# Kernel optimization log

Measured on AMD Instinct MI355X. Metric: run time of the kernel, lower is better.

## Reference

```python
import jax, jax.numpy as jnp
import numpy as np

N = 50000      # total batched graph nodes (both ASTs of all examples)
E = 30000      # edges per edge type
T = 8          # num edge types (no master node, no sibling edges)
H = 128        # gnn hidden = change_vector_dim // 2
TAG = 32       # change-tag embed size
CONTENT = H - TAG
VOCAB = 20000  # rows of token/content encoding table
B = 64         # num examples
STEPS = (3, 3) # layer_time_steps


def setup_inputs() -> dict:
    key = jax.random.key(0)
    ks = jax.random.split(key, 22)
    s = 0.05
    inp = {}
    inp["node_content_ids"] = jax.random.randint(ks[0], (N,), 0, VOCAB)
    inp["node_tag_ids"] = jax.random.randint(ks[1], (N,), 0, 4)
    inp["edge_src"] = jax.random.randint(ks[2], (T, E), 0, N)
    inp["edge_tgt"] = jax.random.randint(ks[3], (T, E), 0, N)
    inp["node2example"] = jnp.sort(jax.random.randint(ks[4], (N,), 0, B))
    inp["content_table"] = jax.random.normal(ks[5], (VOCAB, CONTENT)) * s
    inp["tag_embedding"] = jax.random.normal(ks[6], (4, TAG)) * s
    inp["msg_W"] = jax.random.normal(ks[7], (2, T, H, H)) * s
    inp["msg_b"] = jax.random.normal(ks[8], (2, T, H)) * s
    inp["gru0_Wih"] = jax.random.normal(ks[9], (H, 3 * H)) * s
    inp["gru0_Whh"] = jax.random.normal(ks[10], (H, 3 * H)) * s
    inp["gru0_bih"] = jax.random.normal(ks[11], (3 * H,)) * s
    inp["gru0_bhh"] = jax.random.normal(ks[12], (3 * H,)) * s
    inp["gru1_Wih"] = jax.random.normal(ks[13], (2 * H, 3 * H)) * s  # layer 1 gets residual concat -> 2H input
    inp["gru1_Whh"] = jax.random.normal(ks[14], (H, 3 * H)) * s
    inp["gru1_bih"] = jax.random.normal(ks[15], (3 * H,)) * s
    inp["gru1_bhh"] = jax.random.normal(ks[16], (3 * H,)) * s
    inp["r1_w"] = jax.random.normal(ks[17], (H,)) * s
    inp["r1_b"] = jax.random.normal(ks[18], ()) * s
    inp["r2_w"] = jax.random.normal(ks[19], (H,)) * s
    inp["r2_b"] = jax.random.normal(ks[20], ()) * s
    return inp


def _gru(x, h, Wih, Whh, bih, bhh):
    # PyTorch GRUCell gate order: r, z, n
    gi = x @ Wih + bih
    gh = h @ Whh + bhh
    i_r, i_z, i_n = jnp.split(gi, 3, axis=-1)
    h_r, h_z, h_n = jnp.split(gh, 3, axis=-1)
    r = jax.nn.sigmoid(i_r + h_r)
    z = jax.nn.sigmoid(i_z + h_z)
    n = jnp.tanh(i_n + r * h_n)
    return (1.0 - z) * n + z * h


def reference(node_content_ids, node_tag_ids, edge_src, edge_tgt, node2example,
              content_table, tag_embedding, msg_W, msg_b,
              gru0_Wih, gru0_Whh, gru0_bih, gru0_bhh,
              gru1_Wih, gru1_Whh, gru1_bih, gru1_bhh,
              r1_w, r1_b, r2_w, r2_b):
    # init node embeddings: [token/content encoding || change-tag embedding] -> [N, H]
    init = jnp.concatenate([content_table[node_content_ids],
                            tag_embedding[node_tag_ids]], axis=-1)
    states = init
    layer_out = []
    for layer, steps in enumerate(STEPS):
        for _ in range(steps):
            src_states = states[edge_src]                                   # [T,E,H] gather
            msgs = jnp.einsum('teh,thd->ted', src_states, msg_W[layer]) \
                   + msg_b[layer][:, None, :]                               # per-edge-type linear
            agg = jnp.zeros_like(states).at[edge_tgt].add(msgs)             # scatter-add to targets
            if layer == 1:
                # residual_connections={1:[0]}: concat initial states with incoming messages
                x = jnp.concatenate([init, agg], axis=-1)
                states = _gru(x, states, gru1_Wih, gru1_Whh, gru1_bih, gru1_bhh)
            else:
                states = _gru(agg, states, gru0_Wih, gru0_Whh, gru0_bih, gru0_bhh)
        layer_out.append(states)
    s1, s2 = layer_out
    # gated scalar readout per layer, pooled per example, concatenated -> [B, 2H]
    g1 = jax.nn.sigmoid(s1 @ r1_w + r1_b)[:, None]
    g2 = jax.nn.sigmoid(s2 @ r2_w + r2_b)[:, None]
    pooled1 = jax.ops.segment_sum(g1 * s1, node2example, num_segments=B)
    pooled2 = jax.ops.segment_sum(g2 * s2, node2example, num_segments=B)
    return jnp.concatenate([pooled1, pooled2], axis=-1)
```

## Files before the change

### kernel.cpp

```cpp
#include <hip/hip_runtime.h>
#include <hip/hip_bf16.h>

#define NN 50000
#define NE 30000
#define NT 8
#define HH 128
#define NB 64
#define CONT 96
#define TPB 16
#define EDGES (NT * NE)
#define SBLK 512
#define SNB ((NN + SBLK - 1) / SBLK)
#define RCH 8
#define NTILE (NN / 16)
#define NPAIR ((NTILE + 1) / 2)

typedef __attribute__((ext_vector_type(8))) short short8;
typedef __attribute__((ext_vector_type(4))) float f32x4;

__device__ __forceinline__ float sigm(float x) { return 1.f / (1.f + __expf(-x)); }
__device__ __forceinline__ unsigned short bfbits(float x) {
  __hip_bfloat16 b = __float2bfloat16(x);
  return *(unsigned short*)&b;
}

__global__ __launch_bounds__(256) void init_kernel(
    const int* __restrict__ cid, const int* __restrict__ tg,
    const float* __restrict__ ctab, const float* __restrict__ ttab,
    __hip_bfloat16* __restrict__ sbf, __hip_bfloat16* __restrict__ ibf)
{
  int i = blockIdx.x * 256 + threadIdx.x;
  if (i >= NN * HH) return;
  int n = i >> 7, d = i & 127;
  float v;
  if (d < CONT) v = ctab[(size_t)cid[n] * CONT + d];
  else          v = ttab[(size_t)tg[n] * 32 + (d - CONT)];
  __hip_bfloat16 b = __float2bfloat16(v);
  sbf[i] = b;
  ibf[i] = b;
}

__global__ __launch_bounds__(256) void hist_kernel(
    const int* __restrict__ etgt, int* __restrict__ cnt)
{
  int i = blockIdx.x * 256 + threadIdx.x;
  if (i >= EDGES) return;
  atomicAdd(&cnt[etgt[i]], 1);
}

__global__ __launch_bounds__(SBLK) void scanA_kernel(
    const int* __restrict__ cnt, int* __restrict__ row_ptr, int* __restrict__ bsum)
{
  __shared__ int sm[SBLK];
  const int tid = threadIdx.x;
  const int i = blockIdx.x * SBLK + tid;
  int v = (i < NN) ? cnt[i] : 0;
  sm[tid] = v;
  __syncthreads();
  for (int off = 1; off < SBLK; off <<= 1) {
    int t = (tid >= off) ? sm[tid - off] : 0;
    __syncthreads();
    sm[tid] += t;
    __syncthreads();
  }
  if (i < NN) row_ptr[i] = sm[tid] - v;
  if (tid == SBLK - 1) bsum[blockIdx.x] = sm[tid];
}

__global__ __launch_bounds__(128) void scanB_kernel(
    const int* __restrict__ bsum, int* __restrict__ boff, int* __restrict__ row_ptr)
{
  __shared__ int sm[128];
  const int tid = threadIdx.x;
  int v = (tid < SNB) ? bsum[tid] : 0;
  sm[tid] = v;
  __syncthreads();
  for (int off = 1; off < 128; off <<= 1) {
    int t = (tid >= off) ? sm[tid - off] : 0;
    __syncthreads();
    sm[tid] += t;
    __syncthreads();
  }
  if (tid < SNB) boff[tid] = sm[tid] - v;
  if (tid == 127) row_ptr[NN] = sm[127];
}

__global__ __launch_bounds__(SBLK) void scanC_kernel(
    int* __restrict__ row_ptr, int* __restrict__ cnt2, const int* __restrict__ boff)
{
  int i = blockIdx.x * SBLK + threadIdx.x;
  if (i >= NN) return;
  int r = row_ptr[i] + boff[blockIdx.x];
  row_ptr[i] = r;
  cnt2[i] = r;
}

__global__ __launch_bounds__(256) void scatter_kernel(
    const int* __restrict__ etgt, int* __restrict__ cnt2, int* __restrict__ perm)
{
  int i = blockIdx.x * 256 + threadIdx.x;
  if (i >= EDGES) return;
  perm[i] = atomicAdd(&cnt2[etgt[i]], 1);
}

__global__ __launch_bounds__(128) void exbound_kernel(
    const int* __restrict__ n2e, int* __restrict__ ebnd)
{
  int ex = threadIdx.x;
  if (ex > NB) return;
  int lo = 0, hi = NN;
  while (lo < hi) { int mid = (lo + hi) >> 1; if (n2e[mid] < ex) lo = mid + 1; else hi = mid; }
  ebnd[ex] = lo;
}

__device__ __forceinline__ void gru_swz_one(
    const float* __restrict__ W, __hip_bfloat16* __restrict__ out, int KSL, int mode, int i)
{
  int j = i & 7, lane = (i >> 3) & 63, kk = (i >> 9) % KSL, nt = i / (KSL * 512);
  int hi = lane >> 4, lo = lane & 15;
  int p = kk * 32 + hi * 8 + j;
  int k;
  if (mode == 0)      k = p;
  else if (mode == 1) k = (p & 7) * 16 + (p >> 3);
  else                k = (p < 128) ? p : 128 + ((p - 128) & 7) * 16 + ((p - 128) >> 3);
  out[i] = __float2bfloat16(W[(size_t)k * 384 + nt * 16 + lo]);
}

__global__ __launch_bounds__(256) void wswz_all_kernel(
    const float* __restrict__ msgW, __hip_bfloat16* __restrict__ wswz,
    const float* __restrict__ g0Wih, __hip_bfloat16* __restrict__ w0ih,
    const float* __restrict__ g0Whh, __hip_bfloat16* __restrict__ w0hh,
    const float* __restrict__ g1Wih, __hip_bfloat16* __restrict__ w1ih,
    const float* __restrict__ g1Whh, __hip_bfloat16* __restrict__ w1hh)
{
  int i = blockIdx.x * 256 + threadIdx.x;
  if (i < 262144) {
    int j = i & 7, lane = (i >> 3) & 63, kk = (i >> 9) & 3, nt = (i >> 11) & 7, lt = i >> 14;
    int hi = lane >> 4, lo = lane & 15;
    int k = kk * 32 + hi * 8 + j;
    wswz[i] = __float2bfloat16(msgW[((size_t)lt * HH + k) * HH + nt * 16 + lo]);
    return;
  }
  i -= 262144;
  if (i < 49152)  { gru_swz_one(g0Wih, w0ih, 4, 1, i); return; }
  i -= 49152;
  if (i < 49152)  { gru_swz_one(g0Whh, w0hh, 4, 0, i); return; }
  i -= 49152;
  if (i < 98304)  { gru_swz_one(g1Wih, w1ih, 8, 2, i); return; }
  i -= 98304;
  if (i < 49152)  { gru_swz_one(g1Whh, w1hh, 4, 0, i); return; }
}

__global__ __launch_bounds__(256) void msg_mfma_kernel(
    const __hip_bfloat16* __restrict__ sbf, const int* __restrict__ esrc,
    const int* __restrict__ perm, const __hip_bfloat16* __restrict__ wswz,
    const float* __restrict__ ball, __hip_bfloat16* __restrict__ msgs, int layer)
{
  __shared__ short8 Wl[8 * 4 * 64];
  const int t = blockIdx.y;
  {
    const float4* wg = (const float4*)(wswz + (size_t)(layer * NT + t) * 16384);
    float4* wl = (float4*)Wl;
    for (int i = threadIdx.x; i < 2048; i += 256) wl[i] = wg[i];
  }
  const int lane = threadIdx.x & 63;
  const int wv   = threadIdx.x >> 6;
  const int hi = lane >> 4, lo = lane & 15;
  float bias_v[8];
#pragma unroll
  for (int nt = 0; nt < 8; ++nt)
    bias_v[nt] = ball[(layer * NT + t) * HH + nt * 16 + lo];
  __syncthreads();

  const int tile_end = min((int)(blockIdx.x + 1) * TPB, NE / 16);
  for (int tile = blockIdx.x * TPB + wv; tile < tile_end; tile += 4) {
    const int e0 = tile * 16;
    const int src = esrc[t * NE + e0 + lo];
    const short* srow = (const short*)(sbf + (size_t)src * HH);
    short8 a[4];
#pragma unroll
    for (int kk = 0; kk < 4; ++kk)
      a[kk] = *(const short8*)(srow + kk * 32 + hi * 8);
    int slot[4];
#pragma unroll
    for (int r = 0; r < 4; ++r) slot[r] = perm[t * NE + e0 + hi * 4 + r];
    f32x4 acc[8];
#pragma unroll
    for (int nt = 0; nt < 8; ++nt) acc[nt] = (f32x4){0.f, 0.f, 0.f, 0.f};
#pragma unroll
    for (int nt = 0; nt < 8; ++nt)
#pragma unroll
      for (int kk = 0; kk < 4; ++kk)
        acc[nt] = __builtin_amdgcn_mfma_f32_16x16x32_bf16(
            a[kk], Wl[(nt * 4 + kk) * 64 + lane], acc[nt], 0, 0, 0);
#pragma unroll
    for (int r = 0; r < 4; ++r) {
      short8 m;
#pragma unroll
      for (int nt = 0; nt < 8; ++nt)
        ((unsigned short*)&m)[nt] = bfbits(acc[nt][r] + bias_v[nt]);
      *(short8*)((short*)msgs + (size_t)slot[r] * HH + lo * 8) = m;
    }
  }
}

__global__ __launch_bounds__(256) void reduce_kernel(
    const __hip_bfloat16* __restrict__ msgs, const int* __restrict__ row_ptr,
    __hip_bfloat16* __restrict__ agg)
{
  const int lane = threadIdx.x & 63;
  const int n = blockIdx.x * 4 + (threadIdx.x >> 6);
  if (n >= NN) return;
  const int b = row_ptr[n], e = row_ptr[n + 1];
  float a0 = 0.f, a1 = 0.f;
  for (int i = b; i < e; ++i) {
    unsigned int v = *(const unsigned int*)((const short*)msgs + (size_t)i * HH + lane * 2);
    a0 += __uint_as_float(v << 16);
    a1 += __uint_as_float(v & 0xffff0000u);
  }
  unsigned int o = ((unsigned int)bfbits(a1) << 16) | bfbits(a0);
  *(unsigned int*)((short*)agg + (size_t)n * HH + lane * 2) = o;
}

template <int KSL>
__global__ __launch_bounds__(256) void gru_mfma_kernel(
    const __hip_bfloat16* __restrict__ agg,
    const __hip_bfloat16* __restrict__ ibf,
    const __hip_bfloat16* __restrict__ hbf,
    const __hip_bfloat16* __restrict__ Wih_s,
    const __hip_bfloat16* __restrict__ Whh_s,
    const float* __restrict__ bih, const float* __restrict__ bhh,
    __hip_bfloat16* __restrict__ sbf_out)
{
  __shared__ short8 BihL[2 * 3 * KSL * 64];
  __shared__ short8 BhhL[2 * 3 * 4 * 64];
  const int dtg = blockIdx.y;
  {
    const short8* Bih_g = (const short8*)Wih_s;
    const short8* Bhh_g = (const short8*)Whh_s;
    for (int i = threadIdx.x; i < 2 * 3 * KSL * 64; i += 256) {
      int lane_i = i & 63, kk = (i >> 6) % KSL, g = ((i >> 6) / KSL) % 3, d2 = (i >> 6) / (KSL * 3);
      BihL[i] = Bih_g[((size_t)(dtg * 2 + d2 + 8 * g) * KSL + kk) * 64 + lane_i];
    }
    for (int i = threadIdx.x; i < 2 * 3 * 4 * 64; i += 256) {
      int lane_i = i & 63, kk = (i >> 6) & 3, g = ((i >> 6) >> 2) % 3, d2 = (i >> 6) / 12;
      BhhL[i] = Bhh_g[((size_t)(dtg * 2 + d2 + 8 * g) * 4 + kk) * 64 + lane_i];
    }
  }
  const int lane = threadIdx.x & 63;
  const int wv   = threadIdx.x >> 6;
  const int hi = lane >> 4, lo = lane & 15;
  float birv[2], bizv[2], binv[2], bhrv[2], bhzv[2], bhnv[2];
#pragma unroll
  for (int d2 = 0; d2 < 2; ++d2) {
    const int c = (dtg * 2 + d2) * 16 + lo;
    birv[d2] = bih[c]; bizv[d2] = bih[c + 128]; binv[d2] = bih[c + 256];
    bhrv[d2] = bhh[c]; bhzv[d2] = bhh[c + 128]; bhnv[d2] = bhh[c + 256];
  }
  __syncthreads();

  const int pt = blockIdx.x * 4 + wv;
  if (pt >= NPAIR) return;
  const int t0 = pt * 2;
  const bool two = (t0 + 1 < NTILE);

  short8 ax[2][KSL], ah[2][4];
#pragma unroll
  for (int u = 0; u < 2; ++u) {
    const int nb = ((u && two) ? t0 + 1 : t0) * 16;
    const short* arow = (const short*)(agg + (size_t)(nb + lo) * HH);
    const short* hrow = (const short*)(hbf + (size_t)(nb + lo) * HH);
    if (KSL == 8) {
      const short* irow = (const short*)(ibf + (size_t)(nb + lo) * HH);
#pragma unroll
      for (int kk = 0; kk < 4; ++kk) {
        ax[u][kk]     = *(const short8*)(irow + kk * 32 + hi * 8);
        ax[u][kk + 4] = *(const short8*)(arow + kk * 32 + hi * 8);
      }
    } else {
#pragma unroll
      for (int kk = 0; kk < KSL; ++kk)
        ax[u][kk] = *(const short8*)(arow + kk * 32 + hi * 8);
    }
#pragma unroll
    for (int kk = 0; kk < 4; ++kk)
      ah[u][kk] = *(const short8*)(hrow + kk * 32 + hi * 8);
  }

  f32x4 aR[2][2], aZ[2][2], aNi[2][2], aNh[2][2];
#pragma unroll
  for (int d2 = 0; d2 < 2; ++d2)
#pragma unroll
    for (int u = 0; u < 2; ++u) {
      aR[d2][u] = (f32x4){0.f, 0.f, 0.f, 0.f};
      aZ[d2][u] = (f32x4){0.f, 0.f, 0.f, 0.f};
      aNi[d2][u] = (f32x4){0.f, 0.f, 0.f, 0.f};
      aNh[d2][u] = (f32x4){0.f, 0.f, 0.f, 0.f};
    }

#pragma unroll
  for (int d2 = 0; d2 < 2; ++d2) {
#pragma unroll
    for (int kk = 0; kk < KSL; ++kk) {
      short8 br = BihL[((d2 * 3 + 0) * KSL + kk) * 64 + lane];
      short8 bz = BihL[((d2 * 3 + 1) * KSL + kk) * 64 + lane];
      short8 bn = BihL[((d2 * 3 + 2) * KSL + kk) * 64 + lane];
#pragma unroll
      for (int u = 0; u < 2; ++u) {
        aR[d2][u]  = __builtin_amdgcn_mfma_f32_16x16x32_bf16(ax[u][kk], br, aR[d2][u], 0, 0, 0);
        aZ[d2][u]  = __builtin_amdgcn_mfma_f32_16x16x32_bf16(ax[u][kk], bz, aZ[d2][u], 0, 0, 0);
        aNi[d2][u] = __builtin_amdgcn_mfma_f32_16x16x32_bf16(ax[u][kk], bn, aNi[d2][u], 0, 0, 0);
      }
    }
#pragma unroll
    for (int kk = 0; kk < 4; ++kk) {
      short8 br = BhhL[((d2 * 3 + 0) * 4 + kk) * 64 + lane];
      short8 bz = BhhL[((d2 * 3 + 1) * 4 + kk) * 64 + lane];
      short8 bn = BhhL[((d2 * 3 + 2) * 4 + kk) * 64 + lane];
#pragma unroll
      for (int u = 0; u < 2; ++u) {
        aR[d2][u]  = __builtin_amdgcn_mfma_f32_16x16x32_bf16(ah[u][kk], br, aR[d2][u], 0, 0, 0);
        aZ[d2][u]  = __builtin_amdgcn_mfma_f32_16x16x32_bf16(ah[u][kk], bz, aZ[d2][u], 0, 0, 0);
        aNh[d2][u] = __builtin_amdgcn_mfma_f32_16x16x32_bf16(ah[u][kk], bn, aNh[d2][u], 0, 0, 0);
      }
    }
  }

  const int uend = two ? 2 : 1;
  for (int u = 0; u < uend; ++u) {
    const int nb = (t0 + u) * 16;
#pragma unroll
    for (int d2 = 0; d2 < 2; ++d2) {
      const int c = (dtg * 2 + d2) * 16 + lo;
#pragma unroll
      for (int r = 0; r < 4; ++r) {
        const int node = nb + hi * 4 + r;
        const float rg = sigm(aR[d2][u][r] + birv[d2] + bhrv[d2]);
        const float zg = sigm(aZ[d2][u][r] + bizv[d2] + bhzv[d2]);
        const float ng = tanhf(aNi[d2][u][r] + binv[d2] + rg * (aNh[d2][u][r] + bhnv[d2]));
        const float hc = __bfloat162float(hbf[(size_t)node * HH + c]);
        sbf_out[(size_t)node * HH + c] = __float2bfloat16((1.f - zg) * ng + zg * hc);
      }
    }
  }
}

__global__ __launch_bounds__(256) void readout_kernel(
    const __hip_bfloat16* __restrict__ sbf, const int* __restrict__ ebnd,
    const float* __restrict__ rw, const float* __restrict__ rb,
    float* __restrict__ out, int coff)
{
  __shared__ float sm[4][128];
  const int ex = blockIdx.x / RCH, ch = blockIdx.x % RCH;
  const int s = ebnd[ex], e = ebnd[ex + 1];
  const int lane = threadIdx.x & 63;
  const int wv   = threadIdx.x >> 6;
  const float w0 = rw[2 * lane], w1 = rw[2 * lane + 1], rbv = rb[0];
  float a0 = 0.f, a1 = 0.f;
  for (int n = s + ch * 4 + wv; n < e; n += 4 * RCH) {
    unsigned int v = *(const unsigned int*)((const short*)sbf + (size_t)n * HH + lane * 2);
    const float s0 = __uint_as_float(v << 16);
    const float s1 = __uint_as_float(v & 0xffff0000u);
    float p = s0 * w0 + s1 * w1;
#pragma unroll
    for (int o = 32; o; o >>= 1) p += __shfl_xor(p, o, 64);
    const float g = sigm(p + rbv);
    a0 += g * s0;
    a1 += g * s1;
  }
  sm[wv][2 * lane] = a0;
  sm[wv][2 * lane + 1] = a1;
  __syncthreads();
  if (wv == 0) {
    const int c0 = 2 * lane, c1 = 2 * lane + 1;
    float v0 = sm[0][c0] + sm[1][c0] + sm[2][c0] + sm[3][c0];
    float v1 = sm[0][c1] + sm[1][c1] + sm[2][c1] + sm[3][c1];
    atomicAdd(&out[(size_t)ex * (2 * HH) + coff + c0], v0);
    atomicAdd(&out[(size_t)ex * (2 * HH) + coff + c1], v1);
  }
}

extern "C" void kernel_launch(void* const* d_in, const int* in_sizes, int n_in,
                              void* d_out, int out_size, void* d_ws, size_t ws_size,
                              hipStream_t stream)
{
  const int*   cid   = (const int*)d_in[0];
  const int*   tg    = (const int*)d_in[1];
  const int*   esrc  = (const int*)d_in[2];
  const int*   etgt  = (const int*)d_in[3];
  const int*   n2e   = (const int*)d_in[4];
  const float* ctab  = (const float*)d_in[5];
  const float* ttab  = (const float*)d_in[6];
  const float* msgW  = (const float*)d_in[7];
  const float* msgb  = (const float*)d_in[8];
  const float* g0Wih = (const float*)d_in[9];
  const float* g0Whh = (const float*)d_in[10];
  const float* g0bih = (const float*)d_in[11];
  const float* g0bhh = (const float*)d_in[12];
  const float* g1Wih = (const float*)d_in[13];
  const float* g1Whh = (const float*)d_in[14];
  const float* g1bih = (const float*)d_in[15];
  const float* g1bhh = (const float*)d_in[16];
  const float* r1w   = (const float*)d_in[17];
  const float* r1b   = (const float*)d_in[18];
  const float* r2w   = (const float*)d_in[19];
  const float* r2b   = (const float*)d_in[20];

  float* out = (float*)d_out;
  __hip_bfloat16* sb0  = (__hip_bfloat16*)d_ws;
  __hip_bfloat16* sb1  = sb0 + (size_t)NN * HH;
  __hip_bfloat16* ibf  = sb1 + (size_t)NN * HH;
  __hip_bfloat16* agg  = ibf + (size_t)NN * HH;
  __hip_bfloat16* msgs = agg + (size_t)NN * HH;
  __hip_bfloat16* wswz = msgs + (size_t)EDGES * HH;
  __hip_bfloat16* w0ih = wswz + 262144;
  __hip_bfloat16* w0hh = w0ih + 24 * 4 * 512;
  __hip_bfloat16* w1ih = w0hh + 24 * 4 * 512;
  __hip_bfloat16* w1hh = w1ih + 24 * 8 * 512;
  int* row_ptr = (int*)(w1hh + 24 * 4 * 512);
  int* cnt     = row_ptr + NN + 1;
  int* cnt2    = cnt + NN;
  int* perm    = cnt2 + NN;
  int* bsum    = perm + EDGES;
  int* boff    = bsum + SNB;
  int* ebnd    = boff + SNB;

  hipMemsetAsync(d_out, 0, (size_t)NB * 2 * HH * sizeof(float), stream);
  hipMemsetAsync(cnt, 0, (size_t)NN * sizeof(int), stream);
  const int eblocks = (EDGES + 255) / 256;
  hist_kernel<<<eblocks, 256, 0, stream>>>(etgt, cnt);
  scanA_kernel<<<SNB, SBLK, 0, stream>>>(cnt, row_ptr, bsum);
  scanB_kernel<<<1, 128, 0, stream>>>(bsum, boff, row_ptr);
  scanC_kernel<<<SNB, SBLK, 0, stream>>>(row_ptr, cnt2, boff);
  scatter_kernel<<<eblocks, 256, 0, stream>>>(etgt, cnt2, perm);
  exbound_kernel<<<1, 128, 0, stream>>>(n2e, ebnd);

  wswz_all_kernel<<<507904 / 256, 256, 0, stream>>>(msgW, wswz, g0Wih, w0ih, g0Whh, w0hh,
                                                    g1Wih, w1ih, g1Whh, w1hh);
  init_kernel<<<(NN * HH + 255) / 256, 256, 0, stream>>>(cid, tg, ctab, ttab, sb0, ibf);

  dim3 mgrid((NE / 16 + TPB - 1) / TPB, NT);
  dim3 ggrid((NPAIR + 3) / 4, 4);
  const int rblocks = (NN + 3) / 4;
  __hip_bfloat16* cur = sb0;
  __hip_bfloat16* nxt = sb1;
  for (int s = 0; s < 3; ++s) {
    msg_mfma_kernel<<<mgrid, 256, 0, stream>>>(cur, esrc, perm, wswz, msgb, msgs, 0);
    reduce_kernel<<<rblocks, 256, 0, stream>>>(msgs, row_ptr, agg);
    gru_mfma_kernel<4><<<ggrid, 256, 0, stream>>>(agg, ibf, cur, w0ih, w0hh,
                                                  g0bih, g0bhh, nxt);
    __hip_bfloat16* t = cur; cur = nxt; nxt = t;
  }
  readout_kernel<<<NB * RCH, 256, 0, stream>>>(cur, ebnd, r1w, r1b, out, 0);

  for (int s = 0; s < 3; ++s) {
    msg_mfma_kernel<<<mgrid, 256, 0, stream>>>(cur, esrc, perm, wswz, msgb, msgs, 1);
    reduce_kernel<<<rblocks, 256, 0, stream>>>(msgs, row_ptr, agg);
    gru_mfma_kernel<8><<<ggrid, 256, 0, stream>>>(agg, ibf, cur, w1ih, w1hh,
                                                  g1bih, g1bhh, nxt);
    __hip_bfloat16* t = cur; cur = nxt; nxt = t;
  }
  readout_kernel<<<NB * RCH, 256, 0, stream>>>(cur, ebnd, r2w, r2b, out, HH);
}
```

Baseline: 644.5 us.

## Remap GRU grid for XCD-local weight reuse, read Whh from global, fast tanh

The GRU kernel's 2D grid becomes a 1D grid with a swizzled block index, so consecutive groups of 8 blocks share a row tile and the 4 column-group blocks of a tile are spread in a fixed pattern. The aim is better L2 locality of the node rows across the chiplet dies. The hidden-weight tile is no longer staged in LDS; it is read directly from global memory inside the MFMA loop, which cuts LDS usage and staging cost but adds global loads per wave. tanhf is replaced by an exp-based approximation, which is cheaper but may lose accuracy or overflow for large inputs.

```diff
diff --git a/kernel.cpp b/kernel.cpp
--- a/kernel.cpp
+++ b/kernel.cpp
@@ -14,11 +14,17 @@
 #define RCH 8
 #define NTILE (NN / 16)
 #define NPAIR ((NTILE + 1) / 2)
+#define XB ((NPAIR + 3) / 4)
+#define GGRID ((((XB + 7) / 8)) * 32)
 
 typedef __attribute__((ext_vector_type(8))) short short8;
 typedef __attribute__((ext_vector_type(4))) float f32x4;
 
 __device__ __forceinline__ float sigm(float x) { return 1.f / (1.f + __expf(-x)); }
+__device__ __forceinline__ float tanhf_fast(float x) {
+  float e = __expf(2.f * x);
+  return 1.f - 2.f / (e + 1.f);
+}
 __device__ __forceinline__ unsigned short bfbits(float x) {
   __hip_bfloat16 b = __float2bfloat16(x);
   return *(unsigned short*)&b;
@@ -232,19 +238,17 @@
     const float* __restrict__ bih, const float* __restrict__ bhh,
     __hip_bfloat16* __restrict__ sbf_out)
 {
+  const int wg = blockIdx.x;
+  const int xb = (wg >> 5) * 8 + (wg & 7);
+  const int dtg = (wg >> 3) & 3;
+  if (xb >= XB) return;
+
   __shared__ short8 BihL[2 * 3 * KSL * 64];
-  __shared__ short8 BhhL[2 * 3 * 4 * 64];
-  const int dtg = blockIdx.y;
   {
     const short8* Bih_g = (const short8*)Wih_s;
-    const short8* Bhh_g = (const short8*)Whh_s;
     for (int i = threadIdx.x; i < 2 * 3 * KSL * 64; i += 256) {
       int lane_i = i & 63, kk = (i >> 6) % KSL, g = ((i >> 6) / KSL) % 3, d2 = (i >> 6) / (KSL * 3);
       BihL[i] = Bih_g[((size_t)(dtg * 2 + d2 + 8 * g) * KSL + kk) * 64 + lane_i];
-    }
-    for (int i = threadIdx.x; i < 2 * 3 * 4 * 64; i += 256) {
-      int lane_i = i & 63, kk = (i >> 6) & 3, g = ((i >> 6) >> 2) % 3, d2 = (i >> 6) / 12;
-      BhhL[i] = Bhh_g[((size_t)(dtg * 2 + d2 + 8 * g) * 4 + kk) * 64 + lane_i];
     }
   }
   const int lane = threadIdx.x & 63;
@@ -259,7 +263,7 @@
   }
   __syncthreads();
 
-  const int pt = blockIdx.x * 4 + wv;
+  const int pt = xb * 4 + wv;
   if (pt >= NPAIR) return;
   const int t0 = pt * 2;
   const bool two = (t0 + 1 < NTILE);
@@ -287,6 +291,8 @@
       ah[u][kk] = *(const short8*)(hrow + kk * 32 + hi * 8);
   }
 
+  const short8* __restrict__ Bhh_g = (const short8*)Whh_s;
+
   f32x4 aR[2][2], aZ[2][2], aNi[2][2], aNh[2][2];
 #pragma unroll
   for (int d2 = 0; d2 < 2; ++d2)
@@ -314,9 +320,10 @@
     }
 #pragma unroll
     for (int kk = 0; kk < 4; ++kk) {
-      short8 br = BhhL[((d2 * 3 + 0) * 4 + kk) * 64 + lane];
-      short8 bz = BhhL[((d2 * 3 + 1) * 4 + kk) * 64 + lane];
-      short8 bn = BhhL[((d2 * 3 + 2) * 4 + kk) * 64 + lane];
+      const int dt = dtg * 2 + d2;
+      short8 br = Bhh_g[((size_t)(dt     ) * 4 + kk) * 64 + lane];
+      short8 bz = Bhh_g[((size_t)(dt +  8) * 4 + kk) * 64 + lane];
+      short8 bn = Bhh_g[((size_t)(dt + 16) * 4 + kk) * 64 + lane];
 #pragma unroll
       for (int u = 0; u < 2; ++u) {
         aR[d2][u]  = __builtin_amdgcn_mfma_f32_16x16x32_bf16(ah[u][kk], br, aR[d2][u], 0, 0, 0);
@@ -337,7 +344,7 @@
         const int node = nb + hi * 4 + r;
         const float rg = sigm(aR[d2][u][r] + birv[d2] + bhrv[d2]);
         const float zg = sigm(aZ[d2][u][r] + bizv[d2] + bhzv[d2]);
-        const float ng = tanhf(aNi[d2][u][r] + binv[d2] + rg * (aNh[d2][u][r] + bhnv[d2]));
+        const float ng = tanhf_fast(aNi[d2][u][r] + binv[d2] + rg * (aNh[d2][u][r] + bhnv[d2]));
         const float hc = __bfloat162float(hbf[(size_t)node * HH + c]);
         sbf_out[(size_t)node * HH + c] = __float2bfloat16((1.f - zg) * ng + zg * hc);
       }
@@ -440,14 +447,13 @@
   init_kernel<<<(NN * HH + 255) / 256, 256, 0, stream>>>(cid, tg, ctab, ttab, sb0, ibf);
 
   dim3 mgrid((NE / 16 + TPB - 1) / TPB, NT);
-  dim3 ggrid((NPAIR + 3) / 4, 4);
   const int rblocks = (NN + 3) / 4;
   __hip_bfloat16* cur = sb0;
   __hip_bfloat16* nxt = sb1;
   for (int s = 0; s < 3; ++s) {
     msg_mfma_kernel<<<mgrid, 256, 0, stream>>>(cur, esrc, perm, wswz, msgb, msgs, 0);
     reduce_kernel<<<rblocks, 256, 0, stream>>>(msgs, row_ptr, agg);
-    gru_mfma_kernel<4><<<ggrid, 256, 0, stream>>>(agg, ibf, cur, w0ih, w0hh,
+    gru_mfma_kernel<4><<<GGRID, 256, 0, stream>>>(agg, ibf, cur, w0ih, w0hh,
                                                   g0bih, g0bhh, nxt);
     __hip_bfloat16* t = cur; cur = nxt; nxt = t;
   }
@@ -456,7 +462,7 @@
   for (int s = 0; s < 3; ++s) {
     msg_mfma_kernel<<<mgrid, 256, 0, stream>>>(cur, esrc, perm, wswz, msgb, msgs, 1);
     reduce_kernel<<<rblocks, 256, 0, stream>>>(msgs, row_ptr, agg);
-    gru_mfma_kernel<8><<<ggrid, 256, 0, stream>>>(agg, ibf, cur, w1ih, w1hh,
+    gru_mfma_kernel<8><<<GGRID, 256, 0, stream>>>(agg, ibf, cur, w1ih, w1hh,
                                                   g1bih, g1bhh, nxt);
     __hip_bfloat16* t = cur; cur = nxt; nxt = t;
   }
```

Measured after the change: 591.2 us. 1.09x faster.
